# Optimization experiments

Measured on AMD Instinct MI355X. Metric: run time of the kernel, lower is better.

Reference implementation:

```python
import jax, jax.numpy as jnp
import numpy as np

B, N, E = 4, 20000, 320000
DIN, DMID, DOUT = 64, 64, 32


def setup_inputs() -> dict:
    key = jax.random.key(0)
    ks = jax.random.split(key, 32)
    p = lambda k, shape: jax.random.normal(k, shape, dtype=jnp.float32) * 0.05
    inp = {
        "x": jax.random.normal(ks[0], (B, N, DIN), dtype=jnp.float32),
        "edge_index": jax.random.randint(ks[1], (2, E), 0, N, dtype=jnp.int32),
        "edge_weights": jax.random.uniform(ks[2], (E,), dtype=jnp.float32),
        "prev_hidden_state": jax.random.normal(ks[3], (B, N, DMID), dtype=jnp.float32),
        # GCNConv weights (lin bias=False, separate conv bias) for z/r/h gates
        "Wz": p(ks[4], (DIN, DMID)), "bz": jnp.zeros((DMID,), jnp.float32),
        "Wr": p(ks[5], (DIN, DMID)), "br": jnp.zeros((DMID,), jnp.float32),
        "Wh": p(ks[6], (DIN, DMID)), "bh": jnp.zeros((DMID,), jnp.float32),
        # GRU gate linears: Linear(2*dmid, dmid)
        "Lz": p(ks[7], (2 * DMID, DMID)), "lbz": jnp.zeros((DMID,), jnp.float32),
        "Lr": p(ks[8], (2 * DMID, DMID)), "lbr": jnp.zeros((DMID,), jnp.float32),
        "Lh": p(ks[9], (2 * DMID, DMID)), "lbh": jnp.zeros((DMID,), jnp.float32),
        # GlobalAttention gate_nn: Linear(dmid, 1)
        "gate_w": p(ks[10], (DMID, 1)), "gate_b": jnp.zeros((1,), jnp.float32),
        # head
        "W1": p(ks[11], (DMID, DMID)), "b1": jnp.zeros((DMID,), jnp.float32),
        "W2": p(ks[12], (DMID, DOUT)), "b2": jnp.zeros((DOUT,), jnp.float32),
    }
    return inp


def _gcn(X, W, b, src, dst, norm, n_nodes):
    # X: (B,N,din). GCNConv with add_self_loops=False: scatter(norm * (XW)[src]) + b
    xw = jnp.einsum("bnf,fd->bnd", X, W)              # (B,N,dmid)
    msg = xw[:, src, :] * norm[None, :, None]          # (B,E,dmid)
    agg = jnp.zeros_like(xw).at[:, dst, :].add(msg)    # (B,N,dmid)
    return agg + b


def reference(x, edge_index, edge_weights, prev_hidden_state,
              Wz, bz, Wr, br, Wh, bh,
              Lz, lbz, Lr, lbr, Lh, lbh,
              gate_w, gate_b, W1, b1, W2, b2):
    edge_index = edge_index.reshape(2, -1)
    edge_weights = edge_weights.reshape(-1)
    n_nodes = x.shape[1]
    src, dst = edge_index[0], edge_index[1]

    # symmetric gcn_norm (no self loops): D^-1/2 A D^-1/2
    deg = jnp.zeros((n_nodes,), x.dtype).at[dst].add(edge_weights)
    dinv = jnp.where(deg > 0, jax.lax.rsqrt(jnp.maximum(deg, 1e-12)), 0.0)
    norm = dinv[src] * edge_weights * dinv[dst]

    H = prev_hidden_state
    # TGCN2 GRU-style gates
    Z = jax.nn.sigmoid(jnp.concatenate([_gcn(x, Wz, bz, src, dst, norm, n_nodes), H], -1) @ Lz + lbz)
    R = jax.nn.sigmoid(jnp.concatenate([_gcn(x, Wr, br, src, dst, norm, n_nodes), H], -1) @ Lr + lbr)
    Ht = jnp.tanh(jnp.concatenate([_gcn(x, Wh, bh, src, dst, norm, n_nodes), H * R], -1) @ Lh + lbh)
    H_new = Z * H + (1.0 - Z) * Ht                     # (B,N,dmid)

    # GlobalAttention pooling over nodes per graph
    gate = H_new @ gate_w + gate_b                     # (B,N,1)
    attn = jax.nn.softmax(gate, axis=1)
    y = jnp.sum(attn * H_new, axis=1)                  # (B,dmid)

    y = jax.nn.relu(y @ W1 + b1)
    y = y @ W2 + b2                                    # (B,dout)
    return (y, H_new)
```

## Files before the change

### kernel.cpp

```cpp
#include <hip/hip_runtime.h>
#include <hip/hip_bf16.h>

typedef unsigned short u16;
typedef float f32x4 __attribute__((ext_vector_type(4)));
typedef short s16x8 __attribute__((ext_vector_type(8)));

#define NB 4
#define NN 20000
#define NE 320000
#define ROWS (NB*NN)
#define NBLK 313
#define SLOTCAP 64
#define XTBLK 5000

__device__ __forceinline__ float b2f(u16 u){
  union{unsigned int i; float f;} v; v.i = ((unsigned int)u)<<16; return v.f;
}
__device__ __forceinline__ u16 f2b(float f){
  __hip_bfloat16 h = __float2bfloat16(f);
  return __builtin_bit_cast(u16, h);
}

__global__ void __launch_bounds__(256) setup_kernel(
    const float* __restrict__ x, ushort4* __restrict__ xt4,
    const float* Wz, const float* bz, const float* Lz, const float* lbz,
    const float* Wr, const float* br, const float* Lr, const float* lbr,
    const float* Wh, const float* bh, const float* Lh, const float* lbh,
    int4* __restrict__ wfrag, float* __restrict__ cvec,
    float* __restrict__ deg, int* __restrict__ cursor){
  int bid = blockIdx.x;
  if(bid < XTBLK){
    int t = bid*256 + threadIdx.x;
    int b = t / (NN*16);
    int rem = t - b*(NN*16);
    int n = rem >> 4;
    int c4 = rem & 15;
    float4 v = reinterpret_cast<const float4*>(x)[t];
    ushort4 o; o.x=f2b(v.x); o.y=f2b(v.y); o.z=f2b(v.z); o.w=f2b(v.w);
    xt4[(size_t)n*64 + b*16 + c4] = o;
  } else if(bid < XTBLK+6){
    int m = bid - XTBLK;
    int g = m >> 1, half = m & 1;
    const float* W  = (g==0)?Wz:(g==1)?Wr:Wh;
    const float* L  = (g==0)?Lz:(g==1)?Lr:Lh;
    const float* bb = (g==0)?bz:(g==1)?br:bh;
    const float* lb = (g==0)?lbz:(g==1)?lbr:lbh;
    __shared__ __align__(16) float Wl[4096];
    __shared__ __align__(16) float Lt[4096];
    __shared__ __align__(16) float Pr[4096];
    int t = threadIdx.x;
    if(half == 0){
      for(int i=t; i<1024; i+=256){
        reinterpret_cast<float4*>(Wl)[i] = reinterpret_cast<const float4*>(W)[i];
        reinterpret_cast<float4*>(Lt)[i] = reinterpret_cast<const float4*>(L)[i];
      }
      __syncthreads();
      for(int q=0; q<16; q++){
        int idx = t + 256*q;
        int i = idx>>6, j = idx&63;
        float acc = 0.f;
        for(int k=0;k<64;k++) acc += Wl[i*64+k] * Lt[k*64+j];
        Pr[idx] = acc;
      }
      if(t < 64){
        float a = lb[t];
        for(int k=0;k<64;k++) a += bb[k]*Lt[k*64+t];
        cvec[g*64 + t] = a;
      }
    } else {
      for(int i=t; i<1024; i+=256)
        reinterpret_cast<float4*>(Pr)[i] = reinterpret_cast<const float4*>(L + 4096)[i];
    }
    __syncthreads();
    for(int it=t; it<512; it+=256){
      int l  = it & 63;
      int rl = it >> 6;
      int s  = rl >> 2, tt = rl & 3;
      int k0 = s*32 + (l>>4)*8;
      int n  = tt*16 + (l&15);
      union { u16 v[8]; int4 q4; } tmp;
      #pragma unroll
      for(int j=0;j<8;j++) tmp.v[j] = f2b(Pr[(k0+j)*64 + n]);
      wfrag[m*512 + it] = tmp.q4;
    }
  } else {
    int i = (bid - (XTBLK+6))*256 + threadIdx.x;
    if(i < NN){ deg[i]=0.f; cursor[i]=0; }
  }
}

__global__ void fillslots_kernel(const int* __restrict__ ei, const float* __restrict__ ew,
                                 float* deg, int* cursor, int2* __restrict__ slots){
  int e = blockIdx.x*blockDim.x + threadIdx.x;
  if(e >= NE) return;
  int s = ei[e], d = ei[NE + e];
  float w = ew[e];
  atomicAdd(&deg[d], w);
  int p = atomicAdd(&cursor[d], 1);
  if(p < SLOTCAP){
    int2 ent; ent.x = s; ent.y = __float_as_int(w);
    slots[d*SLOTCAP + p] = ent;
  }
}

__device__ __forceinline__ float dinvf(float d){
  return (d > 0.f) ? rsqrtf(fmaxf(d, 1e-12f)) : 0.f;
}

__global__ void agg_kernel(const ushort4* __restrict__ xt4, const float* __restrict__ deg,
                           const int* __restrict__ cursor, const int2* __restrict__ slots,
                           u16* __restrict__ agg){
  int wave = (blockIdx.x*blockDim.x + threadIdx.x) >> 6;
  int lane = threadIdx.x & 63;
  if(wave >= NN) return;
  int cnt = min(cursor[wave], SLOTCAP);
  float dn = dinvf(deg[wave]);
  const int2* sl = slots + wave*SLOTCAP;
  float a0=0.f, a1=0.f, a2=0.f, a3=0.f;
  int j = 0;
  for(; j+3 < cnt; j+=4){
    int2 ea = sl[j],   eb = sl[j+1];
    int2 ec = sl[j+2], ed = sl[j+3];
    ushort4 va = xt4[(size_t)ea.x*64 + lane];
    ushort4 vb = xt4[(size_t)eb.x*64 + lane];
    ushort4 vc = xt4[(size_t)ec.x*64 + lane];
    ushort4 vd = xt4[(size_t)ed.x*64 + lane];
    float wa = dinvf(deg[ea.x]) * __int_as_float(ea.y) * dn;
    float wb = dinvf(deg[eb.x]) * __int_as_float(eb.y) * dn;
    float wc = dinvf(deg[ec.x]) * __int_as_float(ec.y) * dn;
    float wd = dinvf(deg[ed.x]) * __int_as_float(ed.y) * dn;
    a0 += wa*b2f(va.x) + wb*b2f(vb.x) + wc*b2f(vc.x) + wd*b2f(vd.x);
    a1 += wa*b2f(va.y) + wb*b2f(vb.y) + wc*b2f(vc.y) + wd*b2f(vd.y);
    a2 += wa*b2f(va.z) + wb*b2f(vb.z) + wc*b2f(vc.z) + wd*b2f(vd.z);
    a3 += wa*b2f(va.w) + wb*b2f(vb.w) + wc*b2f(vc.w) + wd*b2f(vd.w);
  }
  for(; j < cnt; j++){
    int2 e = sl[j];
    float w = dinvf(deg[e.x]) * __int_as_float(e.y) * dn;
    ushort4 v = xt4[(size_t)e.x*64 + lane];
    a0 += w * b2f(v.x);
    a1 += w * b2f(v.y);
    a2 += w * b2f(v.z);
    a3 += w * b2f(v.w);
  }
  int b = lane >> 4, c4 = lane & 15;
  ushort4 o; o.x=f2b(a0); o.y=f2b(a1); o.z=f2b(a2); o.w=f2b(a3);
  reinterpret_cast<ushort4*>(agg)[((size_t)b*NN + wave)*16 + c4] = o;
}

#define LDW(m,s,t) __builtin_bit_cast(s16x8, wfrag[((m)*8+(s)*4+(t))*64 + lane])

__global__ void __launch_bounds__(256, 4) gate_kernel(
    const u16* __restrict__ agg, const float* __restrict__ H,
    const int4* __restrict__ wfrag, const float* __restrict__ cvec,
    const float* __restrict__ gate_w, const float* __restrict__ gate_b,
    float* __restrict__ Hnew, float* __restrict__ ypart, float* __restrict__ dpart)
{
  __shared__ __align__(16) u16 rlds[4][1152];
  __shared__ float ylds[4][64];
  __shared__ float dlds[4];

  const int warp = threadIdx.x >> 6, lane = threadIdx.x & 63;
  const int mrow = lane & 15, quad = lane >> 4;
  const int bat = blockIdx.x / NBLK;
  const int blk = blockIdx.x % NBLK;
  const int tin = blk*4 + warp;
  const bool valid = (tin < 1250);
  const int r0 = bat*NN + tin*16;

  float czv[4], crv[4], chv[4], gwv[4];
  #pragma unroll
  for(int t=0;t<4;t++){
    czv[t] = cvec[t*16+mrow];
    crv[t] = cvec[64 + t*16+mrow];
    chv[t] = cvec[128 + t*16+mrow];
    gwv[t] = gate_w[t*16+mrow];
  }
  const float gb = gate_b[0];

  f32x4 Zc[4], Rc[4], Hc[4];
  union { f32x4 v4[2]; float f[8]; } u0, u1;
  if(valid){
    const int4* ap = reinterpret_cast<const int4*>(agg + (size_t)(r0+mrow)*64);
    s16x8 a0 = __builtin_bit_cast(s16x8, ap[quad]);
    s16x8 a1 = __builtin_bit_cast(s16x8, ap[4+quad]);

    const float* Hrow = H + (size_t)(r0+mrow)*64;
    u0.v4[0] = *reinterpret_cast<const f32x4*>(Hrow + quad*8);
    u0.v4[1] = *reinterpret_cast<const f32x4*>(Hrow + quad*8 + 4);
    u1.v4[0] = *reinterpret_cast<const f32x4*>(Hrow + 32 + quad*8);
    u1.v4[1] = *reinterpret_cast<const f32x4*>(Hrow + 32 + quad*8 + 4);
    s16x8 h0, h1;
    #pragma unroll
    for(int j=0;j<8;j++){
      h0[j] = (short)f2b(u0.f[j]);
      h1[j] = (short)f2b(u1.f[j]);
    }

    #pragma unroll
    for(int t=0;t<4;t++){
      f32x4 acc = {0.f,0.f,0.f,0.f};
      acc = __builtin_amdgcn_mfma_f32_16x16x32_bf16(a0, LDW(0,0,t), acc, 0,0,0);
      acc = __builtin_amdgcn_mfma_f32_16x16x32_bf16(a1, LDW(0,1,t), acc, 0,0,0);
      acc = __builtin_amdgcn_mfma_f32_16x16x32_bf16(h0, LDW(1,0,t), acc, 0,0,0);
      acc = __builtin_amdgcn_mfma_f32_16x16x32_bf16(h1, LDW(1,1,t), acc, 0,0,0);
      Zc[t] = acc;
      f32x4 ar = {0.f,0.f,0.f,0.f};
      ar = __builtin_amdgcn_mfma_f32_16x16x32_bf16(a0, LDW(2,0,t), ar, 0,0,0);
      ar = __builtin_amdgcn_mfma_f32_16x16x32_bf16(a1, LDW(2,1,t), ar, 0,0,0);
      ar = __builtin_amdgcn_mfma_f32_16x16x32_bf16(h0, LDW(3,0,t), ar, 0,0,0);
      ar = __builtin_amdgcn_mfma_f32_16x16x32_bf16(h1, LDW(3,1,t), ar, 0,0,0);
      Rc[t] = ar;
      f32x4 ah = {0.f,0.f,0.f,0.f};
      ah = __builtin_amdgcn_mfma_f32_16x16x32_bf16(a0, LDW(4,0,t), ah, 0,0,0);
      ah = __builtin_amdgcn_mfma_f32_16x16x32_bf16(a1, LDW(4,1,t), ah, 0,0,0);
      Hc[t] = ah;
    }

    #pragma unroll
    for(int t=0;t<4;t++){
      #pragma unroll
      for(int i=0;i<4;i++){
        float r = 1.f/(1.f + __expf(-(Rc[t][i] + crv[t])));
        rlds[warp][(quad*4+i)*72 + t*16 + mrow] = f2b(r);
      }
    }
    const u16* rp = &rlds[warp][mrow*72 + quad*8];
    int4 rv0 = *reinterpret_cast<const int4*>(rp);
    int4 rv1 = *reinterpret_cast<const int4*>(rp + 32);
    const u16* rv0p = reinterpret_cast<const u16*>(&rv0);
    const u16* rv1p = reinterpret_cast<const u16*>(&rv1);
    s16x8 hr0, hr1;
    #pragma unroll
    for(int j=0;j<8;j++){
      hr0[j] = (short)f2b(u0.f[j] * b2f(rv0p[j]));
      hr1[j] = (short)f2b(u1.f[j] * b2f(rv1p[j]));
    }
    #pragma unroll
    for(int t=0;t<4;t++){
      Hc[t] = __builtin_amdgcn_mfma_f32_16x16x32_bf16(hr0, LDW(5,0,t), Hc[t], 0,0,0);
      Hc[t] = __builtin_amdgcn_mfma_f32_16x16x32_bf16(hr1, LDW(5,1,t), Hc[t], 0,0,0);
    }

    float hnv[4][4];
    float ga[4] = {0.f,0.f,0.f,0.f};
    #pragma unroll
    for(int t=0;t<4;t++){
      #pragma unroll
      for(int i=0;i<4;i++){
        int row = r0 + quad*4 + i, col = t*16 + mrow;
        float z  = 1.f/(1.f + __expf(-(Zc[t][i] + czv[t])));
        float ht = tanhf(Hc[t][i] + chv[t]);
        float hv = H[(size_t)row*64 + col];
        float hn = z*hv + (1.f - z)*ht;
        Hnew[(size_t)row*64 + col] = hn;
        hnv[t][i] = hn;
        ga[i] += hn * gwv[t];
      }
    }
    #pragma unroll
    for(int i=0;i<4;i++){
      float v = ga[i];
      v += __shfl_xor(v, 1, 64);
      v += __shfl_xor(v, 2, 64);
      v += __shfl_xor(v, 4, 64);
      v += __shfl_xor(v, 8, 64);
      ga[i] = v;
    }
    float e_[4]; float dsum = 0.f;
    #pragma unroll
    for(int i=0;i<4;i++){ e_[i] = __expf(ga[i] + gb); dsum += e_[i]; }
    #pragma unroll
    for(int t=0;t<4;t++){
      float s = 0.f;
      #pragma unroll
      for(int i=0;i<4;i++) s += e_[i]*hnv[t][i];
      s += __shfl_xor(s, 16, 64);
      s += __shfl_xor(s, 32, 64);
      if(lane < 16) ylds[warp][t*16 + mrow] = s;
    }
    dsum += __shfl_xor(dsum, 16, 64);
    dsum += __shfl_xor(dsum, 32, 64);
    if(lane == 0) dlds[warp] = dsum;
  } else {
    if(lane < 16){
      #pragma unroll
      for(int t=0;t<4;t++) ylds[warp][t*16 + mrow] = 0.f;
    }
    if(lane == 0) dlds[warp] = 0.f;
  }
  __syncthreads();
  int t = threadIdx.x;
  if(t < 64){
    float s = ylds[0][t] + ylds[1][t] + ylds[2][t] + ylds[3][t];
    ypart[(size_t)blockIdx.x*64 + t] = s;
  }
  if(t == 64) dpart[blockIdx.x] = dlds[0] + dlds[1] + dlds[2] + dlds[3];
}

__global__ void __launch_bounds__(256) head_kernel(
    const float* __restrict__ ypart, const float* __restrict__ dpart,
    const float* W1, const float* b1,
    const float* W2, const float* b2, float* out){
  __shared__ float red[4][64];
  __shared__ float yv[64];
  __shared__ float hid[64];
  __shared__ float dshared;
  int b = blockIdx.x, t = threadIdx.x;
  int d = t & 63, q = t >> 6;
  const float* yp = ypart + (size_t)b*NBLK*64;
  float s = 0.f;
  #pragma unroll 4
  for(int k=q; k<NBLK; k+=4) s += yp[k*64 + d];
  red[q][d] = s;
  if(t < 64){
    const float* dp = dpart + b*NBLK;
    float ds = 0.f;
    for(int k=t; k<NBLK; k+=64) ds += dp[k];
    ds += __shfl_xor(ds, 1, 64);
    ds += __shfl_xor(ds, 2, 64);
    ds += __shfl_xor(ds, 4, 64);
    ds += __shfl_xor(ds, 8, 64);
    ds += __shfl_xor(ds, 16, 64);
    ds += __shfl_xor(ds, 32, 64);
    if(t == 0) dshared = ds;
  }
  __syncthreads();
  if(t < 64) yv[t] = red[0][t] + red[1][t] + red[2][t] + red[3][t];
  __syncthreads();
  if(t < 64){
    float inv = 1.f / dshared;
    float acc = b1[t];
    #pragma unroll 4
    for(int k=0;k<64;k++) acc += (yv[k]*inv) * W1[k*64+t];
    hid[t] = fmaxf(acc, 0.f);
  }
  __syncthreads();
  if(t < 32){
    float a2 = b2[t];
    #pragma unroll 4
    for(int d2=0; d2<64; d2++) a2 += hid[d2] * W2[d2*32+t];
    out[b*32+t] = a2;
  }
}

extern "C" void kernel_launch(void* const* d_in, const int* in_sizes, int n_in,
                              void* d_out, int out_size, void* d_ws, size_t ws_size,
                              hipStream_t stream) {
  const float* x   = (const float*)d_in[0];
  const int*   ei  = (const int*)d_in[1];
  const float* ew  = (const float*)d_in[2];
  const float* H   = (const float*)d_in[3];
  const float* Wz = (const float*)d_in[4],  *bz = (const float*)d_in[5];
  const float* Wr = (const float*)d_in[6],  *br = (const float*)d_in[7];
  const float* Wh = (const float*)d_in[8],  *bh = (const float*)d_in[9];
  const float* Lz = (const float*)d_in[10], *lbz = (const float*)d_in[11];
  const float* Lr = (const float*)d_in[12], *lbr = (const float*)d_in[13];
  const float* Lh = (const float*)d_in[14], *lbh = (const float*)d_in[15];
  const float* gw = (const float*)d_in[16], *gbp = (const float*)d_in[17];
  const float* W1 = (const float*)d_in[18], *b1 = (const float*)d_in[19];
  const float* W2 = (const float*)d_in[20], *b2 = (const float*)d_in[21];

  float* y_out    = (float*)d_out;
  float* Hnew_out = (float*)d_out + 128;

  char* ws = (char*)d_ws;
  size_t off = 0;
  auto alloc = [&](size_t bytes)->char*{
    off = (off + 255) & ~(size_t)255;
    char* p = ws + off; off += bytes; return p;
  };
  float*   deg      = (float*)alloc(NN*4);
  int*     cursor   = (int*)  alloc(NN*4);
  int2*    slots    = (int2*) alloc((size_t)NN*SLOTCAP*8);
  ushort4* xt4      = (ushort4*)alloc((size_t)NN*256*2);
  u16*     agg      = (u16*)  alloc((size_t)ROWS*64*2);
  int4*    wfrag    = (int4*) alloc(3072*16);
  float*   cvec     = (float*)alloc(192*4);
  float*   ypart    = (float*)alloc((size_t)NB*NBLK*64*4);
  float*   dpart    = (float*)alloc((size_t)NB*NBLK*4);
  (void)ws_size; (void)n_in; (void)in_sizes; (void)out_size;

  const int zeroblk = (NN + 255)/256;
  setup_kernel<<<XTBLK + 6 + zeroblk, 256, 0, stream>>>(
      x, xt4, Wz,bz,Lz,lbz, Wr,br,Lr,lbr, Wh,bh,Lh,lbh, wfrag, cvec, deg, cursor);
  fillslots_kernel<<<(NE+255)/256, 256, 0, stream>>>(ei, ew, deg, cursor, slots);
  agg_kernel<<<(NN+3)/4, 256, 0, stream>>>(xt4, deg, cursor, slots, agg);
  gate_kernel<<<NB*NBLK, 256, 0, stream>>>(agg, H, wfrag, cvec, gw, gbp, Hnew_out, ypart, dpart);
  head_kernel<<<4, 256, 0, stream>>>(ypart, dpart, W1, b1, W2, b2, y_out);
}
```

Baseline: 232.9 us.

## Fuse neighbor aggregation into gate kernel via shared-memory staging

```diff
diff --git a/kernel.cpp b/kernel.cpp
--- a/kernel.cpp
+++ b/kernel.cpp
@@ -9,7 +9,7 @@
 #define NN 20000
 #define NE 320000
 #define ROWS (NB*NN)
-#define NBLK 313
+#define GBLK 1250
 #define SLOTCAP 64
 #define XTBLK 5000
 
@@ -107,66 +107,63 @@
   return (d > 0.f) ? rsqrtf(fmaxf(d, 1e-12f)) : 0.f;
 }
 
-__global__ void agg_kernel(const ushort4* __restrict__ xt4, const float* __restrict__ deg,
-                           const int* __restrict__ cursor, const int2* __restrict__ slots,
-                           u16* __restrict__ agg){
-  int wave = (blockIdx.x*blockDim.x + threadIdx.x) >> 6;
-  int lane = threadIdx.x & 63;
-  if(wave >= NN) return;
-  int cnt = min(cursor[wave], SLOTCAP);
-  float dn = dinvf(deg[wave]);
-  const int2* sl = slots + wave*SLOTCAP;
-  float a0=0.f, a1=0.f, a2=0.f, a3=0.f;
-  int j = 0;
-  for(; j+3 < cnt; j+=4){
-    int2 ea = sl[j],   eb = sl[j+1];
-    int2 ec = sl[j+2], ed = sl[j+3];
-    ushort4 va = xt4[(size_t)ea.x*64 + lane];
-    ushort4 vb = xt4[(size_t)eb.x*64 + lane];
-    ushort4 vc = xt4[(size_t)ec.x*64 + lane];
-    ushort4 vd = xt4[(size_t)ed.x*64 + lane];
-    float wa = dinvf(deg[ea.x]) * __int_as_float(ea.y) * dn;
-    float wb = dinvf(deg[eb.x]) * __int_as_float(eb.y) * dn;
-    float wc = dinvf(deg[ec.x]) * __int_as_float(ec.y) * dn;
-    float wd = dinvf(deg[ed.x]) * __int_as_float(ed.y) * dn;
-    a0 += wa*b2f(va.x) + wb*b2f(vb.x) + wc*b2f(vc.x) + wd*b2f(vd.x);
-    a1 += wa*b2f(va.y) + wb*b2f(vb.y) + wc*b2f(vc.y) + wd*b2f(vd.y);
-    a2 += wa*b2f(va.z) + wb*b2f(vb.z) + wc*b2f(vc.z) + wd*b2f(vd.z);
-    a3 += wa*b2f(va.w) + wb*b2f(vb.w) + wc*b2f(vc.w) + wd*b2f(vd.w);
-  }
-  for(; j < cnt; j++){
-    int2 e = sl[j];
-    float w = dinvf(deg[e.x]) * __int_as_float(e.y) * dn;
-    ushort4 v = xt4[(size_t)e.x*64 + lane];
-    a0 += w * b2f(v.x);
-    a1 += w * b2f(v.y);
-    a2 += w * b2f(v.z);
-    a3 += w * b2f(v.w);
-  }
-  int b = lane >> 4, c4 = lane & 15;
-  ushort4 o; o.x=f2b(a0); o.y=f2b(a1); o.z=f2b(a2); o.w=f2b(a3);
-  reinterpret_cast<ushort4*>(agg)[((size_t)b*NN + wave)*16 + c4] = o;
-}
-
 #define LDW(m,s,t) __builtin_bit_cast(s16x8, wfrag[((m)*8+(s)*4+(t))*64 + lane])
 
 __global__ void __launch_bounds__(256, 4) gate_kernel(
-    const u16* __restrict__ agg, const float* __restrict__ H,
+    const ushort4* __restrict__ xt4, const float* __restrict__ deg,
+    const int* __restrict__ cursor, const int2* __restrict__ slots,
+    const float* __restrict__ H,
     const int4* __restrict__ wfrag, const float* __restrict__ cvec,
     const float* __restrict__ gate_w, const float* __restrict__ gate_b,
     float* __restrict__ Hnew, float* __restrict__ ypart, float* __restrict__ dpart)
 {
+  __shared__ ushort4 aglds[16][64];
   __shared__ __align__(16) u16 rlds[4][1152];
   __shared__ float ylds[4][64];
   __shared__ float dlds[4];
 
   const int warp = threadIdx.x >> 6, lane = threadIdx.x & 63;
   const int mrow = lane & 15, quad = lane >> 4;
-  const int bat = blockIdx.x / NBLK;
-  const int blk = blockIdx.x % NBLK;
-  const int tin = blk*4 + warp;
-  const bool valid = (tin < 1250);
-  const int r0 = bat*NN + tin*16;
+  const int blk = blockIdx.x;
+  const int n0 = blk*16;
+
+  #pragma unroll
+  for(int i=0;i<4;i++){
+    int nl = warp*4 + i;
+    int node = n0 + nl;
+    int cnt = min(cursor[node], SLOTCAP);
+    float dn = dinvf(deg[node]);
+    const int2* sl = slots + node*SLOTCAP;
+    float a0=0.f, a1=0.f, a2=0.f, a3=0.f;
+    int j = 0;
+    for(; j+3 < cnt; j+=4){
+      int2 ea = sl[j],   eb = sl[j+1];
+      int2 ec = sl[j+2], ed = sl[j+3];
+      ushort4 va = xt4[(size_t)ea.x*64 + lane];
+      ushort4 vb = xt4[(size_t)eb.x*64 + lane];
+      ushort4 vc = xt4[(size_t)ec.x*64 + lane];
+      ushort4 vd = xt4[(size_t)ed.x*64 + lane];
+      float wa = dinvf(deg[ea.x]) * __int_as_float(ea.y) * dn;
+      float wb = dinvf(deg[eb.x]) * __int_as_float(eb.y) * dn;
+      float wc = dinvf(deg[ec.x]) * __int_as_float(ec.y) * dn;
+      float wd = dinvf(deg[ed.x]) * __int_as_float(ed.y) * dn;
+      a0 += wa*b2f(va.x) + wb*b2f(vb.x) + wc*b2f(vc.x) + wd*b2f(vd.x);
+      a1 += wa*b2f(va.y) + wb*b2f(vb.y) + wc*b2f(vc.y) + wd*b2f(vd.y);
+      a2 += wa*b2f(va.z) + wb*b2f(vb.z) + wc*b2f(vc.z) + wd*b2f(vd.z);
+      a3 += wa*b2f(va.w) + wb*b2f(vb.w) + wc*b2f(vc.w) + wd*b2f(vd.w);
+    }
+    for(; j < cnt; j++){
+      int2 e = sl[j];
+      float w = dinvf(deg[e.x]) * __int_as_float(e.y) * dn;
+      ushort4 v = xt4[(size_t)e.x*64 + lane];
+      a0 += w * b2f(v.x);
+      a1 += w * b2f(v.y);
+      a2 += w * b2f(v.z);
+      a3 += w * b2f(v.w);
+    }
+    ushort4 o; o.x=f2b(a0); o.y=f2b(a1); o.z=f2b(a2); o.w=f2b(a3);
+    aglds[nl][lane] = o;
+  }
 
   float czv[4], crv[4], chv[4], gwv[4];
   #pragma unroll
@@ -177,125 +174,119 @@
     gwv[t] = gate_w[t*16+mrow];
   }
   const float gb = gate_b[0];
+  __syncthreads();
+
+  const int r0 = warp*NN + n0;
+
+  s16x8 a0 = __builtin_bit_cast(s16x8, *reinterpret_cast<const int4*>(&aglds[mrow][warp*16 + quad*2]));
+  s16x8 a1 = __builtin_bit_cast(s16x8, *reinterpret_cast<const int4*>(&aglds[mrow][warp*16 + 8 + quad*2]));
+
+  const float* Hrow = H + (size_t)(r0+mrow)*64;
+  union { f32x4 v4[2]; float f[8]; } u0, u1;
+  u0.v4[0] = *reinterpret_cast<const f32x4*>(Hrow + quad*8);
+  u0.v4[1] = *reinterpret_cast<const f32x4*>(Hrow + quad*8 + 4);
+  u1.v4[0] = *reinterpret_cast<const f32x4*>(Hrow + 32 + quad*8);
+  u1.v4[1] = *reinterpret_cast<const f32x4*>(Hrow + 32 + quad*8 + 4);
+  s16x8 h0, h1;
+  #pragma unroll
+  for(int j=0;j<8;j++){
+    h0[j] = (short)f2b(u0.f[j]);
+    h1[j] = (short)f2b(u1.f[j]);
+  }
 
   f32x4 Zc[4], Rc[4], Hc[4];
-  union { f32x4 v4[2]; float f[8]; } u0, u1;
-  if(valid){
-    const int4* ap = reinterpret_cast<const int4*>(agg + (size_t)(r0+mrow)*64);
-    s16x8 a0 = __builtin_bit_cast(s16x8, ap[quad]);
-    s16x8 a1 = __builtin_bit_cast(s16x8, ap[4+quad]);
-
-    const float* Hrow = H + (size_t)(r0+mrow)*64;
-    u0.v4[0] = *reinterpret_cast<const f32x4*>(Hrow + quad*8);
-    u0.v4[1] = *reinterpret_cast<const f32x4*>(Hrow + quad*8 + 4);
-    u1.v4[0] = *reinterpret_cast<const f32x4*>(Hrow + 32 + quad*8);
-    u1.v4[1] = *reinterpret_cast<const f32x4*>(Hrow + 32 + quad*8 + 4);
-    s16x8 h0, h1;
-    #pragma unroll
-    for(int j=0;j<8;j++){
-      h0[j] = (short)f2b(u0.f[j]);
-      h1[j] = (short)f2b(u1.f[j]);
-    }
-
-    #pragma unroll
-    for(int t=0;t<4;t++){
-      f32x4 acc = {0.f,0.f,0.f,0.f};
-      acc = __builtin_amdgcn_mfma_f32_16x16x32_bf16(a0, LDW(0,0,t), acc, 0,0,0);
-      acc = __builtin_amdgcn_mfma_f32_16x16x32_bf16(a1, LDW(0,1,t), acc, 0,0,0);
-      acc = __builtin_amdgcn_mfma_f32_16x16x32_bf16(h0, LDW(1,0,t), acc, 0,0,0);
-      acc = __builtin_amdgcn_mfma_f32_16x16x32_bf16(h1, LDW(1,1,t), acc, 0,0,0);
-      Zc[t] = acc;
-      f32x4 ar = {0.f,0.f,0.f,0.f};
-      ar = __builtin_amdgcn_mfma_f32_16x16x32_bf16(a0, LDW(2,0,t), ar, 0,0,0);
-      ar = __builtin_amdgcn_mfma_f32_16x16x32_bf16(a1, LDW(2,1,t), ar, 0,0,0);
-      ar = __builtin_amdgcn_mfma_f32_16x16x32_bf16(h0, LDW(3,0,t), ar, 0,0,0);
-      ar = __builtin_amdgcn_mfma_f32_16x16x32_bf16(h1, LDW(3,1,t), ar, 0,0,0);
-      Rc[t] = ar;
-      f32x4 ah = {0.f,0.f,0.f,0.f};
-      ah = __builtin_amdgcn_mfma_f32_16x16x32_bf16(a0, LDW(4,0,t), ah, 0,0,0);
-      ah = __builtin_amdgcn_mfma_f32_16x16x32_bf16(a1, LDW(4,1,t), ah, 0,0,0);
-      Hc[t] = ah;
-    }
-
-    #pragma unroll
-    for(int t=0;t<4;t++){
-      #pragma unroll
-      for(int i=0;i<4;i++){
-        float r = 1.f/(1.f + __expf(-(Rc[t][i] + crv[t])));
-        rlds[warp][(quad*4+i)*72 + t*16 + mrow] = f2b(r);
-      }
-    }
-    const u16* rp = &rlds[warp][mrow*72 + quad*8];
-    int4 rv0 = *reinterpret_cast<const int4*>(rp);
-    int4 rv1 = *reinterpret_cast<const int4*>(rp + 32);
-    const u16* rv0p = reinterpret_cast<const u16*>(&rv0);
-    const u16* rv1p = reinterpret_cast<const u16*>(&rv1);
-    s16x8 hr0, hr1;
-    #pragma unroll
-    for(int j=0;j<8;j++){
-      hr0[j] = (short)f2b(u0.f[j] * b2f(rv0p[j]));
-      hr1[j] = (short)f2b(u1.f[j] * b2f(rv1p[j]));
-    }
-    #pragma unroll
-    for(int t=0;t<4;t++){
-      Hc[t] = __builtin_amdgcn_mfma_f32_16x16x32_bf16(hr0, LDW(5,0,t), Hc[t], 0,0,0);
-      Hc[t] = __builtin_amdgcn_mfma_f32_16x16x32_bf16(hr1, LDW(5,1,t), Hc[t], 0,0,0);
-    }
-
-    float hnv[4][4];
-    float ga[4] = {0.f,0.f,0.f,0.f};
-    #pragma unroll
-    for(int t=0;t<4;t++){
-      #pragma unroll
-      for(int i=0;i<4;i++){
-        int row = r0 + quad*4 + i, col = t*16 + mrow;
-        float z  = 1.f/(1.f + __expf(-(Zc[t][i] + czv[t])));
-        float ht = tanhf(Hc[t][i] + chv[t]);
-        float hv = H[(size_t)row*64 + col];
-        float hn = z*hv + (1.f - z)*ht;
-        Hnew[(size_t)row*64 + col] = hn;
-        hnv[t][i] = hn;
-        ga[i] += hn * gwv[t];
-      }
-    }
+  #pragma unroll
+  for(int t=0;t<4;t++){
+    f32x4 acc = {0.f,0.f,0.f,0.f};
+    acc = __builtin_amdgcn_mfma_f32_16x16x32_bf16(a0, LDW(0,0,t), acc, 0,0,0);
+    acc = __builtin_amdgcn_mfma_f32_16x16x32_bf16(a1, LDW(0,1,t), acc, 0,0,0);
+    acc = __builtin_amdgcn_mfma_f32_16x16x32_bf16(h0, LDW(1,0,t), acc, 0,0,0);
+    acc = __builtin_amdgcn_mfma_f32_16x16x32_bf16(h1, LDW(1,1,t), acc, 0,0,0);
+    Zc[t] = acc;
+    f32x4 ar = {0.f,0.f,0.f,0.f};
+    ar = __builtin_amdgcn_mfma_f32_16x16x32_bf16(a0, LDW(2,0,t), ar, 0,0,0);
+    ar = __builtin_amdgcn_mfma_f32_16x16x32_bf16(a1, LDW(2,1,t), ar, 0,0,0);
+    ar = __builtin_amdgcn_mfma_f32_16x16x32_bf16(h0, LDW(3,0,t), ar, 0,0,0);
+    ar = __builtin_amdgcn_mfma_f32_16x16x32_bf16(h1, LDW(3,1,t), ar, 0,0,0);
+    Rc[t] = ar;
+    f32x4 ah = {0.f,0.f,0.f,0.f};
+    ah = __builtin_amdgcn_mfma_f32_16x16x32_bf16(a0, LDW(4,0,t), ah, 0,0,0);
+    ah = __builtin_amdgcn_mfma_f32_16x16x32_bf16(a1, LDW(4,1,t), ah, 0,0,0);
+    Hc[t] = ah;
+  }
+
+  #pragma unroll
+  for(int t=0;t<4;t++){
     #pragma unroll
     for(int i=0;i<4;i++){
-      float v = ga[i];
-      v += __shfl_xor(v, 1, 64);
-      v += __shfl_xor(v, 2, 64);
-      v += __shfl_xor(v, 4, 64);
-      v += __shfl_xor(v, 8, 64);
-      ga[i] = v;
-    }
-    float e_[4]; float dsum = 0.f;
+      float r = 1.f/(1.f + __expf(-(Rc[t][i] + crv[t])));
+      rlds[warp][(quad*4+i)*72 + t*16 + mrow] = f2b(r);
+    }
+  }
+  const u16* rp = &rlds[warp][mrow*72 + quad*8];
+  int4 rv0 = *reinterpret_cast<const int4*>(rp);
+  int4 rv1 = *reinterpret_cast<const int4*>(rp + 32);
+  const u16* rv0p = reinterpret_cast<const u16*>(&rv0);
+  const u16* rv1p = reinterpret_cast<const u16*>(&rv1);
+  s16x8 hr0, hr1;
+  #pragma unroll
+  for(int j=0;j<8;j++){
+    hr0[j] = (short)f2b(u0.f[j] * b2f(rv0p[j]));
+    hr1[j] = (short)f2b(u1.f[j] * b2f(rv1p[j]));
+  }
+  #pragma unroll
+  for(int t=0;t<4;t++){
+    Hc[t] = __builtin_amdgcn_mfma_f32_16x16x32_bf16(hr0, LDW(5,0,t), Hc[t], 0,0,0);
+    Hc[t] = __builtin_amdgcn_mfma_f32_16x16x32_bf16(hr1, LDW(5,1,t), Hc[t], 0,0,0);
+  }
+
+  float hnv[4][4];
+  float ga[4] = {0.f,0.f,0.f,0.f};
+  #pragma unroll
+  for(int t=0;t<4;t++){
     #pragma unroll
-    for(int i=0;i<4;i++){ e_[i] = __expf(ga[i] + gb); dsum += e_[i]; }
+    for(int i=0;i<4;i++){
+      int row = r0 + quad*4 + i, col = t*16 + mrow;
+      float z  = 1.f/(1.f + __expf(-(Zc[t][i] + czv[t])));
+      float ht = tanhf(Hc[t][i] + chv[t]);
+      float hv = H[(size_t)row*64 + col];
+      float hn = z*hv + (1.f - z)*ht;
+      Hnew[(size_t)row*64 + col] = hn;
+      hnv[t][i] = hn;
+      ga[i] += hn * gwv[t];
+    }
+  }
+  #pragma unroll
+  for(int i=0;i<4;i++){
+    float v = ga[i];
+    v += __shfl_xor(v, 1, 64);
+    v += __shfl_xor(v, 2, 64);
+    v += __shfl_xor(v, 4, 64);
+    v += __shfl_xor(v, 8, 64);
+    ga[i] = v;
+  }
+  float e_[4]; float dsum = 0.f;
+  #pragma unroll
+  for(int i=0;i<4;i++){ e_[i] = __expf(ga[i] + gb); dsum += e_[i]; }
+  #pragma unroll
+  for(int t=0;t<4;t++){
+    float s = 0.f;
     #pragma unroll
-    for(int t=0;t<4;t++){
-      float s = 0.f;
-      #pragma unroll
-      for(int i=0;i<4;i++) s += e_[i]*hnv[t][i];
-      s += __shfl_xor(s, 16, 64);
-      s += __shfl_xor(s, 32, 64);
-      if(lane < 16) ylds[warp][t*16 + mrow] = s;
-    }
-    dsum += __shfl_xor(dsum, 16, 64);
-    dsum += __shfl_xor(dsum, 32, 64);
-    if(lane == 0) dlds[warp] = dsum;
-  } else {
-    if(lane < 16){
-      #pragma unroll
-      for(int t=0;t<4;t++) ylds[warp][t*16 + mrow] = 0.f;
-    }
-    if(lane == 0) dlds[warp] = 0.f;
-  }
+    for(int i=0;i<4;i++) s += e_[i]*hnv[t][i];
+    s += __shfl_xor(s, 16, 64);
+    s += __shfl_xor(s, 32, 64);
+    if(lane < 16) ylds[warp][t*16 + mrow] = s;
+  }
+  dsum += __shfl_xor(dsum, 16, 64);
+  dsum += __shfl_xor(dsum, 32, 64);
+  if(lane == 0) dlds[warp] = dsum;
   __syncthreads();
   int t = threadIdx.x;
-  if(t < 64){
-    float s = ylds[0][t] + ylds[1][t] + ylds[2][t] + ylds[3][t];
-    ypart[(size_t)blockIdx.x*64 + t] = s;
-  }
-  if(t == 64) dpart[blockIdx.x] = dlds[0] + dlds[1] + dlds[2] + dlds[3];
+  {
+    int wb = t >> 6, col = t & 63;
+    ypart[((size_t)wb*GBLK + blk)*64 + col] = ylds[wb][col];
+  }
+  if(t < 4) dpart[t*GBLK + blk] = dlds[t];
 }
 
 __global__ void __launch_bounds__(256) head_kernel(
@@ -308,15 +299,15 @@
   __shared__ float dshared;
   int b = blockIdx.x, t = threadIdx.x;
   int d = t & 63, q = t >> 6;
-  const float* yp = ypart + (size_t)b*NBLK*64;
+  const float* yp = ypart + (size_t)b*GBLK*64;
   float s = 0.f;
   #pragma unroll 4
-  for(int k=q; k<NBLK; k+=4) s += yp[k*64 + d];
+  for(int k=q; k<GBLK; k+=4) s += yp[k*64 + d];
   red[q][d] = s;
   if(t < 64){
-    const float* dp = dpart + b*NBLK;
+    const float* dp = dpart + b*GBLK;
     float ds = 0.f;
-    for(int k=t; k<NBLK; k+=64) ds += dp[k];
+    for(int k=t; k<GBLK; k+=64) ds += dp[k];
     ds += __shfl_xor(ds, 1, 64);
     ds += __shfl_xor(ds, 2, 64);
     ds += __shfl_xor(ds, 4, 64);
@@ -374,18 +365,17 @@
   int*     cursor   = (int*)  alloc(NN*4);
   int2*    slots    = (int2*) alloc((size_t)NN*SLOTCAP*8);
   ushort4* xt4      = (ushort4*)alloc((size_t)NN*256*2);
-  u16*     agg      = (u16*)  alloc((size_t)ROWS*64*2);
   int4*    wfrag    = (int4*) alloc(3072*16);
   float*   cvec     = (float*)alloc(192*4);
-  float*   ypart    = (float*)alloc((size_t)NB*NBLK*64*4);
-  float*   dpart    = (float*)alloc((size_t)NB*NBLK*4);
+  float*   ypart    = (float*)alloc((size_t)NB*GBLK*64*4);
+  float*   dpart    = (float*)alloc((size_t)NB*GBLK*4);
   (void)ws_size; (void)n_in; (void)in_sizes; (void)out_size;
 
   const int zeroblk = (NN + 255)/256;
   setup_kernel<<<XTBLK + 6 + zeroblk, 256, 0, stream>>>(
       x, xt4, Wz,bz,Lz,lbz, Wr,br,Lr,lbr, Wh,bh,Lh,lbh, wfrag, cvec, deg, cursor);
   fillslots_kernel<<<(NE+255)/256, 256, 0, stream>>>(ei, ew, deg, cursor, slots);
-  agg_kernel<<<(NN+3)/4, 256, 0, stream>>>(xt4, deg, cursor, slots, agg);
-  gate_kernel<<<NB*NBLK, 256, 0, stream>>>(agg, H, wfrag, cvec, gw, gbp, Hnew_out, ypart, dpart);
+  gate_kernel<<<GBLK, 256, 0, stream>>>(xt4, deg, cursor, slots, H, wfrag, cvec,
+                                        gw, gbp, Hnew_out, ypart, dpart);
   head_kernel<<<4, 256, 0, stream>>>(ypart, dpart, W1, b1, W2, b2, y_out);
 }
```

Result: slower. 266.1 us (+14.2%).
